# Kernel tuning notes

Measured on AMD Instinct MI355X. Metric: run time of the kernel, lower is better.

Reference implementation:

```python
import jax, jax.numpy as jnp
import numpy as np

N = 20000        # atoms
NEIGH = 12       # neighbors per atom
BSTEPS = 40      # bond GBF steps, range [0, 8]
ASTEPS = 20      # angle GBF steps, range [-1, 1]
H = 64           # hidden size
NCLS = 2         # n_classification
NCRYS = 20       # crystals (contiguous blocks of 1000 atoms)
NREL = 3         # edge relation types


def gbf(data, dmin, dmax, steps):
    # Gaussian basis expansion: exp(-(d - mu)^2 / gamma^2), gamma = (max-min)/steps
    filters = jnp.linspace(dmin, dmax, steps)
    gamma = (dmax - dmin) / steps
    return jnp.exp(-((data[..., None] - filters) ** 2) / gamma ** 2)


def rgcn(x, src, dst, etype, W_rel, W_root, b):
    # RGCNConv (PyG default): out = x @ W_root + b + sum_r mean_{j in N_r(i)} x_j @ W_r
    out = x @ W_root + b
    for r in range(NREL):
        w = (etype == r).astype(x.dtype)                     # [E]
        msg = (x @ W_rel[r])[src] * w[:, None]               # transform-then-gather: [E, H]
        s = jax.ops.segment_sum(msg, dst, num_segments=x.shape[0])
        c = jax.ops.segment_sum(w, dst, num_segments=x.shape[0])
        out = out + s / jnp.maximum(c, 1.0)[:, None]
    return out


def _forward(bond_fea, angle_fea, species, nbr_idx, crys_idx,
             W1b_rel, W1b_root, b1b, W1a_rel, W1a_root, b1a,
             W2b_rel, W2b_root, b2b, W2a_rel, W2a_root, b2a,
             fc_W, fc_b):
    n = bond_fea.shape[0]
    src = jnp.repeat(jnp.arange(n, dtype=jnp.int32), NEIGH)  # edge sources
    dst = nbr_idx.reshape(-1)                                # edge targets
    etype = species[src] + species[dst]                      # 0/1/2 per species pair

    edge_fea = gbf(bond_fea, 0.0, 8.0, BSTEPS).reshape(n, -1)      # [N, 480]
    ang_fea = gbf(angle_fea, -1.0, 1.0, ASTEPS).reshape(n, -1)     # [N, 2880]

    bf = jax.nn.relu(rgcn(edge_fea, src, dst, etype, W1b_rel, W1b_root, b1b))
    af = jax.nn.relu(rgcn(ang_fea, src, dst, etype, W1a_rel, W1a_root, b1a))
    # dropout treated as identity (eval/deterministic reference)
    bf = jax.nn.relu(rgcn(bf, src, dst, etype, W2b_rel, W2b_root, b2b))
    af = jax.nn.relu(rgcn(af, src, dst, etype, W2a_rel, W2a_root, b2a))

    feat = jnp.concatenate([bf, af], axis=1)                 # [N, 128]

    # pool: mean over contiguous [start, end) ranges per crystal
    starts = crys_idx[:, 0]
    crys_id = jnp.searchsorted(starts, jnp.arange(n), side='right') - 1
    sums = jax.ops.segment_sum(feat, crys_id, num_segments=NCRYS)
    counts = (crys_idx[:, 1] - crys_idx[:, 0]).astype(feat.dtype)[:, None]
    pooled = sums / counts                                   # [NCRYS, 128]

    return pooled @ fc_W + fc_b                              # [NCRYS, NCLS]


def setup_inputs() -> dict:
    key = jax.random.key(0)
    ks = jax.random.split(key, 20)
    bond_fea = jax.random.uniform(ks[0], (N, NEIGH), dtype=jnp.float32) * 8.0
    angle_fea = jax.random.uniform(ks[1], (N, NEIGH, NEIGH), dtype=jnp.float32) * 2.0 - 1.0
    species = jax.random.randint(ks[2], (N,), 0, 2, dtype=jnp.int32)
    nbr_idx = jax.random.randint(ks[3], (N, NEIGH), 0, N, dtype=jnp.int32)
    starts = jnp.arange(NCRYS, dtype=jnp.int32) * (N // NCRYS)
    crys_idx = jnp.stack([starts, starts + (N // NCRYS)], axis=1)

    def w(k, shape, fan_in):
        return jax.random.normal(k, shape, dtype=jnp.float32) / np.sqrt(fan_in)

    in_b = BSTEPS * NEIGH            # 480
    in_a = ASTEPS * NEIGH * NEIGH    # 2880
    return {
        'bond_fea': bond_fea, 'angle_fea': angle_fea, 'species': species,
        'nbr_idx': nbr_idx, 'crys_idx': crys_idx,
        'W1b_rel': w(ks[4], (NREL, in_b, H), in_b), 'W1b_root': w(ks[5], (in_b, H), in_b),
        'b1b': jnp.zeros((H,), jnp.float32),
        'W1a_rel': w(ks[6], (NREL, in_a, H), in_a), 'W1a_root': w(ks[7], (in_a, H), in_a),
        'b1a': jnp.zeros((H,), jnp.float32),
        'W2b_rel': w(ks[8], (NREL, H, H), H), 'W2b_root': w(ks[9], (H, H), H),
        'b2b': jnp.zeros((H,), jnp.float32),
        'W2a_rel': w(ks[10], (NREL, H, H), H), 'W2a_root': w(ks[11], (H, H), H),
        'b2a': jnp.zeros((H,), jnp.float32),
        'fc_W': w(ks[12], (2 * H, NCLS), 2 * H), 'fc_b': jnp.zeros((NCLS,), jnp.float32),
    }


def reference(bond_fea, angle_fea, species, nbr_idx, crys_idx,
              W1b_rel, W1b_root, b1b, W1a_rel, W1a_root, b1a,
              W2b_rel, W2b_root, b2b, W2a_rel, W2a_root, b2a,
              fc_W, fc_b):
    return _forward(bond_fea, angle_fea, species, nbr_idx, crys_idx,
                    W1b_rel, W1b_root, b1b, W1a_rel, W1a_root, b1a,
                    W2b_rel, W2b_root, b2b, W2a_rel, W2a_root, b2a,
                    fc_W, fc_b)
```

## Files before the change

kernel.cpp:

```cpp
#include <hip/hip_runtime.h>

#define NN 20000
#define NNP 20096
#define NEIGH 12
#define NCRYS 20
#define MT2 1256
#define NSUB 16

typedef __bf16 bf16x8 __attribute__((ext_vector_type(8)));
typedef __bf16 bf16x4 __attribute__((ext_vector_type(4)));
typedef float f32x4 __attribute__((ext_vector_type(4)));

__device__ __forceinline__ void pack_one(const float* Wrel, const float* Wroot,
                                         __bf16* Wp, int K, int idx) {
    int k = idx >> 8, n = idx & 255;
    int r = n >> 6, h = n & 63;
    float v = (r < 3) ? Wrel[((size_t)r * K + k) * 64 + h] : Wroot[(size_t)k * 64 + h];
    int kt = k >> 5, k8 = (k >> 3) & 3, j = k & 7, nt = n >> 4, ni = n & 15;
    Wp[((((size_t)kt * 16 + nt) * 4 + k8) * 16 + ni) * 8 + j] = (__bf16)v;
}

__device__ __forceinline__ void pack_cat(const float* Wrel, const float* Wroot,
                                         __bf16* Wp, int idx) {
    int k4 = idx >> 6, n = idx & 63;
    int q = k4 >> 6, kk = k4 & 63;
    float v = q ? Wrel[(((q - 1) * 64 + kk) * 64) + n] : Wroot[kk * 64 + n];
    int kt = k4 >> 5, k8 = (k4 >> 3) & 3, j = k4 & 7, nt = n >> 4, ni = n & 15;
    Wp[((((size_t)kt * 4 + nt) * 4 + k8) * 16 + ni) * 8 + j] = (__bf16)v;
}

__global__ __launch_bounds__(256) void setup_kernel(
    const int* __restrict__ species, const int* __restrict__ nbr,
    int* __restrict__ adj, int* __restrict__ deg,
    const float* __restrict__ W1b_rel, const float* __restrict__ W1b_root,
    const float* __restrict__ W1a_rel, const float* __restrict__ W1a_root,
    const float* __restrict__ W2b_rel, const float* __restrict__ W2b_root,
    const float* __restrict__ W2a_rel, const float* __restrict__ W2a_root,
    __bf16* __restrict__ Wp1b, __bf16* __restrict__ Wp1a,
    __bf16* __restrict__ Wp2b, __bf16* __restrict__ Wp2a,
    const float* __restrict__ bond, const float* __restrict__ angle,
    float* __restrict__ bondT, float* __restrict__ angleT) {
    __shared__ float ls[64 * 145];
    const int bx = blockIdx.x, tid = threadIdx.x;
    if (bx < 938) {
        int e = bx * 256 + tid;
        if (e < NN * NEIGH) {
            int i = e / NEIGH;
            int d = nbr[e];
            int r = species[i] + species[d];
            int slot = atomicAdd(&deg[d], 1);
            if (slot < 64) adj[(size_t)d * 64 + slot] = i | (r << 28);
        }
    } else if (bx < 938 + 256) {
        const int S0 = 480 * 256;
        const int S1 = S0 + 2880 * 256;
        const int S2 = S1 + 16384;
        const int S3 = S2 + 16384;
        const int S4 = S3 + 8192;
        const int S5 = S4 + 16384;
        for (int idx = (bx - 938) * 256 + tid; idx < S5; idx += 256 * 256) {
            if (idx < S0)       pack_one(W1b_rel, W1b_root, Wp1b, 480, idx);
            else if (idx < S1)  pack_one(W1a_rel, W1a_root, Wp1a, 2880, idx - S0);
            else if (idx < S2)  pack_cat(W2b_rel, W2b_root, Wp2b, idx - S1);
            else if (idx < S3)  pack_cat(W2a_rel, W2a_root, Wp2a, idx - S2);
            else if (idx < S4)  Wp1b[480 * 256 + (idx - S3)] = (__bf16)0.f;
            else                Wp1a[2880 * 256 + (idx - S4)] = (__bf16)0.f;
        }
    } else {
        int tb = bx - 1194;
        if (tb < 314) {
            int m0 = tb * 64;
            for (int idx = tid; idx < 64 * 144; idx += 256) {
                int mm = idx / 144, j = idx - mm * 144;
                int m = m0 + mm;
                ls[mm * 145 + j] = (m < NN) ? angle[(size_t)m * 144 + j] : 0.f;
            }
            __syncthreads();
            for (int idx = tid; idx < 148 * 64; idx += 256) {
                int j = idx >> 6, mm = idx & 63;
                angleT[(size_t)j * NNP + m0 + mm] = (j < 144) ? ls[mm * 145 + j] : 0.f;
            }
        } else {
            int m0 = (tb - 314) * 64;
            for (int idx = tid; idx < 64 * 12; idx += 256) {
                int mm = idx / 12, j = idx - mm * 12;
                int m = m0 + mm;
                ls[mm * 13 + j] = (m < NN) ? bond[(size_t)m * 12 + j] : 0.f;
            }
            __syncthreads();
            for (int idx = tid; idx < 16 * 64; idx += 256) {
                int j = idx >> 6, mm = idx & 63;
                bondT[(size_t)j * NNP + m0 + mm] = (j < 12) ? ls[mm * 13 + j] : 0.f;
            }
        }
    }
}

template <int MODE>
__device__ __forceinline__ void gemm1_body(const float* __restrict__ xT,
                                           const __bf16* __restrict__ Wp,
                                           __bf16* __restrict__ Y, int mb,
                                           __bf16* __restrict__ Al) {
    constexpr int KTOT = (MODE == 0) ? 512 : 2944;
    constexpr int NPH = KTOT / 64;
    constexpr int DIVN = (MODE == 0) ? 40 : 20;
    constexpr int ADDJ = 64 / DIVN;
    constexpr int ADDS = 64 % DIVN;
    constexpr float F0 = (MODE == 0) ? 0.f : -1.f;
    constexpr float FS = (MODE == 0) ? (8.f / 39.f) : (2.f / 19.f);
    constexpr float NG2 = ((MODE == 0) ? -25.f : -100.f) * 1.44269504f;
    const float C  = __builtin_amdgcn_exp2f(2.f * NG2 * FS * FS);
    const float P1 = NG2 * FS * FS;
    const float P2 = -2.f * NG2 * FS;

    const int tid = threadIdx.x;
    const int lane = tid & 63, wv = tid >> 6;
    const int m0 = mb * 64;
    const int smt = tid >> 7;
    const int sk8 = (tid >> 5) & 3;
    const int smi = (tid >> 1) & 15;
    const int sjh = (tid & 1) * 4;
    const int sgm = m0 + smt * 16 + smi;
    const int kk0 = sk8 * 8 + sjh;
    const int swoff = (((smt * 4 + sk8) * 16 + smi) * 8 + sjh);
    const int k8b = lane >> 4, nib = lane & 15;

    f32x4 acc[4][2] = {};

    const float* pA0 = xT + (size_t)(kk0 / DIVN) * NNP + sgm;
    const float* pA1 = xT + (size_t)((32 + kk0) / DIVN) * NNP + sgm;
    int sL0 = kk0 % DIVN, sL1 = (32 + kk0) % DIVN;
    int sS0 = sL0, sS1 = sL1;

    const bf16x8* pB0 = (const bf16x8*)Wp + ((size_t)(2 * wv) * 4 + k8b) * 16 + nib;
    const bf16x8* pB1 = pB0 + 1024;

    bf16x8 bEv[4], bOd[4];

    auto advL = [&]() {
        sL0 += ADDS;
        if (sL0 >= DIVN) { sL0 -= DIVN; pA0 += (size_t)(ADDJ + 1) * NNP; } else pA0 += (size_t)ADDJ * NNP;
        sL1 += ADDS;
        if (sL1 >= DIVN) { sL1 -= DIVN; pA1 += (size_t)(ADDJ + 1) * NNP; } else pA1 += (size_t)ADDJ * NNP;
    };
    auto advS = [&]() {
        sS0 += ADDS; if (sS0 >= DIVN) sS0 -= DIVN;
        sS1 += ADDS; if (sS1 >= DIVN) sS1 -= DIVN;
    };
    auto loadB = [&](bf16x8* d) {
        d[0] = pB0[0]; d[1] = pB0[64]; d[2] = pB1[0]; d[3] = pB1[64];
        pB0 += 2048; pB1 += 2048;
    };
    auto stage = [&](float a0, float a1, __bf16* dst) {
        float d0 = a0 - (F0 + (float)sS0 * FS);
        float d1 = a1 - (F0 + (float)sS1 * FS);
        float e0a = __builtin_amdgcn_exp2f(NG2 * d0 * d0);
        float q0a = __builtin_amdgcn_exp2f(fmaf(P2, d0, P1));
        float e0b = __builtin_amdgcn_exp2f(NG2 * d1 * d1);
        float q0b = __builtin_amdgcn_exp2f(fmaf(P2, d1, P1));
        float e1a = e0a * q0a, q1a = q0a * C;
        float e2a = e1a * q1a, e3a = e2a * q1a * C;
        float e1b = e0b * q0b, q1b = q0b * C;
        float e2b = e1b * q1b, e3b = e2b * q1b * C;
        bf16x4 v0, v1;
        v0[0] = (__bf16)e0a; v0[1] = (__bf16)e1a; v0[2] = (__bf16)e2a; v0[3] = (__bf16)e3a;
        v1[0] = (__bf16)e0b; v1[1] = (__bf16)e1b; v1[2] = (__bf16)e2b; v1[3] = (__bf16)e3b;
        *(bf16x4*)&dst[swoff] = v0;
        *(bf16x4*)&dst[2048 + swoff] = v1;
    };
    auto mma = [&](const __bf16* Ab, const bf16x8* bc) {
        bf16x8 af[4], ag[4];
#pragma unroll
        for (int t4 = 0; t4 < 4; ++t4) {
            af[t4] = *(const bf16x8*)&Ab[(((((t4 << 2) + k8b) << 4) + nib) << 3)];
            ag[t4] = *(const bf16x8*)&Ab[2048 + (((((t4 << 2) + k8b) << 4) + nib) << 3)];
        }
#pragma unroll
        for (int i = 0; i < 4; ++i) {
            acc[i][0] = __builtin_amdgcn_mfma_f32_16x16x32_bf16(af[i], bc[0], acc[i][0], 0, 0, 0);
            acc[i][1] = __builtin_amdgcn_mfma_f32_16x16x32_bf16(af[i], bc[1], acc[i][1], 0, 0, 0);
        }
#pragma unroll
        for (int i = 0; i < 4; ++i) {
            acc[i][0] = __builtin_amdgcn_mfma_f32_16x16x32_bf16(ag[i], bc[2], acc[i][0], 0, 0, 0);
            acc[i][1] = __builtin_amdgcn_mfma_f32_16x16x32_bf16(ag[i], bc[3], acc[i][1], 0, 0, 0);
        }
    };

    float a00 = pA0[0], a01 = pA1[0]; advL();
    float aN0 = pA0[0], aN1 = pA1[0]; advL();
    stage(a00, a01, Al); advS();
    loadB(bEv);
    loadB(bOd);
    __syncthreads();

    for (int p2 = 0; p2 < NPH / 2; ++p2) {
        const bool last = (p2 == NPH / 2 - 1);
        mma(Al, bEv);
        if (!last) loadB(bEv);
        stage(aN0, aN1, Al + 4096); advS();
        if (!last) { aN0 = pA0[0]; aN1 = pA1[0]; advL(); }
        __syncthreads();
        mma(Al + 4096, bOd);
        if (!last) {
            loadB(bOd);
            stage(aN0, aN1, Al); advS();
            aN0 = pA0[0]; aN1 = pA1[0]; advL();
        }
        __syncthreads();
    }

    const int mrow0 = m0 + ((lane >> 4) << 2);
    const int ncol = (wv << 5) + nib;
#pragma unroll
    for (int i = 0; i < 4; ++i)
#pragma unroll
        for (int j = 0; j < 2; ++j)
#pragma unroll
            for (int v = 0; v < 4; ++v) {
                int m = mrow0 + i * 16 + v;
                if (m < NN) Y[(size_t)m * 256 + ncol + j * 16] = (__bf16)acc[i][j][v];
            }
}

__global__ __launch_bounds__(512, 4) void mega_gemm1(const float* __restrict__ bondT,
                                                     const float* __restrict__ angleT,
                                                     const __bf16* __restrict__ Wp1b,
                                                     const __bf16* __restrict__ Wp1a,
                                                     __bf16* __restrict__ Yb, __bf16* __restrict__ Ya) {
    __shared__ __align__(16) __bf16 Al[2 * 4096];
    int bx = blockIdx.x;
    if (bx < 314) gemm1_body<1>(angleT, Wp1a, Ya, bx, Al);
    else          gemm1_body<0>(bondT, Wp1b, Yb, bx - 314, Al);
}

__device__ __forceinline__ float agg_node(const __bf16* __restrict__ Y,
                                          const int* __restrict__ adj,
                                          const int* __restrict__ deg,
                                          const float* __restrict__ bias,
                                          int node, int h) {
    int dg = min(deg[node], 64);
    int e = adj[(size_t)node * 64 + h];
    bool val = h < dg;
    int r = e >> 28;
    unsigned long long bl0 = __ballot(val && r == 0);
    unsigned long long bl1 = __ballot(val && r == 1);
    unsigned long long bl2 = __ballot(val && r == 2);
    int c0 = __popcll(bl0), c1 = __popcll(bl1), c2 = __popcll(bl2);
    float s0 = 0.f, s1 = 0.f, s2 = 0.f;
    if (dg > 0) {
        int e0 = __builtin_amdgcn_readfirstlane(e);
        int ec = val ? e : e0;
        for (int k0 = 0; k0 < dg; k0 += 16) {
            float v[16];
#pragma unroll
            for (int i = 0; i < 16; ++i) {
                int ek = __builtin_amdgcn_readlane(ec, k0 + i);
                v[i] = (float)Y[(size_t)(ek & 0x0FFFFFFF) * 256 + (ek >> 28) * 64 + h];
            }
#pragma unroll
            for (int i = 0; i < 16; ++i) {
                int kk = k0 + i;
                if (kk < dg) {
                    int rr = __builtin_amdgcn_readlane(ec, kk) >> 28;
                    if (rr == 0) s0 += v[i];
                    else if (rr == 1) s1 += v[i];
                    else s2 += v[i];
                }
            }
        }
    }
    float o = (float)Y[(size_t)node * 256 + 192 + h] + bias[h] +
              s0 / fmaxf((float)c0, 1.f) + s1 / fmaxf((float)c1, 1.f) +
              s2 / fmaxf((float)c2, 1.f);
    return fmaxf(o, 0.f);
}

__global__ __launch_bounds__(256) void agg_packed(const __bf16* __restrict__ Yb,
                                                  const __bf16* __restrict__ Ya,
                                                  const int* __restrict__ adj,
                                                  const int* __restrict__ deg,
                                                  const float* __restrict__ biasb,
                                                  const float* __restrict__ biasa,
                                                  __bf16* __restrict__ outb,
                                                  __bf16* __restrict__ outa) {
    const __bf16* Y = blockIdx.y ? Ya : Yb;
    const float* bias = blockIdx.y ? biasa : biasb;
    __bf16* outp = blockIdx.y ? outa : outb;
    int node = blockIdx.x * 4 + (threadIdx.x >> 6);
    int h = threadIdx.x & 63;
    if (node >= NN) return;
    float o = agg_node(Y, adj, deg, bias, node, h);
    outp[(size_t)node * 64 + h] = (__bf16)o;
}

__global__ __launch_bounds__(256) void agg2(const __bf16* __restrict__ Hb,
                                            const __bf16* __restrict__ Ha,
                                            const int* __restrict__ adj,
                                            const int* __restrict__ deg,
                                            __bf16* __restrict__ Apb,
                                            __bf16* __restrict__ Apa) {
    const __bf16* H = blockIdx.y ? Ha : Hb;
    __bf16* Ap = blockIdx.y ? Apa : Apb;
    int node = blockIdx.x * 4 + (threadIdx.x >> 6);
    int h = threadIdx.x & 63;
    float hd = 0.f, r0 = 0.f, r1 = 0.f, r2 = 0.f;
    if (node < NN) {
        int dg = min(deg[node], 64);
        int e = adj[(size_t)node * 64 + h];
        bool val = h < dg;
        int r = e >> 28;
        unsigned long long bl0 = __ballot(val && r == 0);
        unsigned long long bl1 = __ballot(val && r == 1);
        unsigned long long bl2 = __ballot(val && r == 2);
        int c0 = __popcll(bl0), c1 = __popcll(bl1), c2 = __popcll(bl2);
        float s0 = 0.f, s1 = 0.f, s2 = 0.f;
        hd = (float)H[(size_t)node * 64 + h];
        if (dg > 0) {
            int e0 = __builtin_amdgcn_readfirstlane(e);
            int ec = val ? e : e0;
            for (int k0 = 0; k0 < dg; k0 += 16) {
                float v[16];
#pragma unroll
                for (int i = 0; i < 16; ++i) {
                    int ek = __builtin_amdgcn_readlane(ec, k0 + i);
                    v[i] = (float)H[(size_t)(ek & 0x0FFFFFFF) * 64 + h];
                }
#pragma unroll
                for (int i = 0; i < 16; ++i) {
                    int kk = k0 + i;
                    if (kk < dg) {
                        int rr = __builtin_amdgcn_readlane(ec, kk) >> 28;
                        if (rr == 0) s0 += v[i];
                        else if (rr == 1) s1 += v[i];
                        else s2 += v[i];
                    }
                }
            }
        }
        r0 = s0 / fmaxf((float)c0, 1.f);
        r1 = s1 / fmaxf((float)c1, 1.f);
        r2 = s2 / fmaxf((float)c2, 1.f);
    }
    int mt = node >> 4, mi = node & 15;
    float vals[4] = {hd, r0, r1, r2};
#pragma unroll
    for (int q = 0; q < 4; ++q) {
        int K4 = q * 64 + h;
        int kt = K4 >> 5, k8 = (K4 >> 3) & 3, j = K4 & 7;
        Ap[((((size_t)kt * MT2 + mt) * 4 + k8) * 16 + mi) * 8 + j] = (__bf16)vals[q];
    }
}

__global__ __launch_bounds__(256) void gemm3(const __bf16* __restrict__ Apb,
                                             const __bf16* __restrict__ Apa,
                                             const __bf16* __restrict__ Wpb,
                                             const __bf16* __restrict__ Wpa,
                                             const float* __restrict__ bb,
                                             const float* __restrict__ ba,
                                             const int* __restrict__ crys,
                                             float* __restrict__ pooled) {
    const int ch = blockIdx.y;
    const bf16x8* Ag = (const bf16x8*)(ch ? Apa : Apb);
    const bf16x8* Bg = (const bf16x8*)(ch ? Wpa : Wpb);
    const float* bias = ch ? ba : bb;
    const int base = ch ? 64 : 0;
    const int tid = threadIdx.x, lane = tid & 63, wv = tid >> 6;
    const int mt0 = blockIdx.x * 8 + wv * 2;
    const int k8b = lane >> 4, nib = lane & 15;
    f32x4 acc[2][4] = {};
#pragma unroll
    for (int kt = 0; kt < 8; ++kt) {
        bf16x8 a0 = Ag[(((size_t)kt * MT2 + mt0) * 4 + k8b) * 16 + nib];
        bf16x8 a1 = Ag[(((size_t)kt * MT2 + mt0 + 1) * 4 + k8b) * 16 + nib];
        bf16x8 b0 = Bg[(((size_t)kt * 4 + 0) * 4 + k8b) * 16 + nib];
        bf16x8 b1 = Bg[(((size_t)kt * 4 + 1) * 4 + k8b) * 16 + nib];
        bf16x8 b2 = Bg[(((size_t)kt * 4 + 2) * 4 + k8b) * 16 + nib];
        bf16x8 b3 = Bg[(((size_t)kt * 4 + 3) * 4 + k8b) * 16 + nib];
        acc[0][0] = __builtin_amdgcn_mfma_f32_16x16x32_bf16(a0, b0, acc[0][0], 0, 0, 0);
        acc[0][1] = __builtin_amdgcn_mfma_f32_16x16x32_bf16(a0, b1, acc[0][1], 0, 0, 0);
        acc[0][2] = __builtin_amdgcn_mfma_f32_16x16x32_bf16(a0, b2, acc[0][2], 0, 0, 0);
        acc[0][3] = __builtin_amdgcn_mfma_f32_16x16x32_bf16(a0, b3, acc[0][3], 0, 0, 0);
        acc[1][0] = __builtin_amdgcn_mfma_f32_16x16x32_bf16(a1, b0, acc[1][0], 0, 0, 0);
        acc[1][1] = __builtin_amdgcn_mfma_f32_16x16x32_bf16(a1, b1, acc[1][1], 0, 0, 0);
        acc[1][2] = __builtin_amdgcn_mfma_f32_16x16x32_bf16(a1, b2, acc[1][2], 0, 0, 0);
        acc[1][3] = __builtin_amdgcn_mfma_f32_16x16x32_bf16(a1, b3, acc[1][3], 0, 0, 0);
    }
    const int rowoff = ((lane >> 4) << 2);
#pragma unroll
    for (int i = 0; i < 2; ++i)
#pragma unroll
        for (int v = 0; v < 4; ++v) {
            int m = (mt0 + i) * 16 + rowoff + v;
            if (m < NN) {
                int cc = 0;
#pragma unroll
                for (int t = 1; t < NCRYS; ++t) cc += (m >= crys[t * 2]) ? 1 : 0;
                int sub = ((m >> 4) + ((m >> 2) & 3)) & (NSUB - 1);
                float* pb = &pooled[((size_t)cc * NSUB + sub) * 128 + base];
#pragma unroll
                for (int j = 0; j < 4; ++j) {
                    int n = j * 16 + nib;
                    float o = fmaxf(acc[i][j][v] + bias[n], 0.f);
                    atomicAdd(&pb[n], o);
                }
            }
        }
}

__global__ void final2(const float* __restrict__ pooled, const int* __restrict__ crys,
                       const float* __restrict__ fcW, const float* __restrict__ fcb,
                       float* __restrict__ out) {
    int c = blockIdx.x >> 1, o = blockIdx.x & 1;
    int l = threadIdx.x;
    float cnt = (float)(crys[c * 2 + 1] - crys[c * 2]);
    float sb = 0.f, sa = 0.f;
    for (int s = 0; s < NSUB; ++s) {
        sb += pooled[((size_t)c * NSUB + s) * 128 + l];
        sa += pooled[((size_t)c * NSUB + s) * 128 + 64 + l];
    }
    float a = sb * fcW[l * 2 + o] + sa * fcW[(64 + l) * 2 + o];
    for (int s = 32; s > 0; s >>= 1) a += __shfl_down(a, s);
    if (l == 0) out[c * 2 + o] = a / cnt + fcb[o];
}

extern "C" void kernel_launch(void* const* d_in, const int* in_sizes, int n_in,
                              void* d_out, int out_size, void* d_ws, size_t ws_size,
                              hipStream_t stream) {
    const float* bond    = (const float*)d_in[0];
    const float* angle   = (const float*)d_in[1];
    const int*   species = (const int*)d_in[2];
    const int*   nbr     = (const int*)d_in[3];
    const int*   crys    = (const int*)d_in[4];
    const float* W1b_rel = (const float*)d_in[5];
    const float* W1b_root= (const float*)d_in[6];
    const float* b1b     = (const float*)d_in[7];
    const float* W1a_rel = (const float*)d_in[8];
    const float* W1a_root= (const float*)d_in[9];
    const float* b1a     = (const float*)d_in[10];
    const float* W2b_rel = (const float*)d_in[11];
    const float* W2b_root= (const float*)d_in[12];
    const float* b2b     = (const float*)d_in[13];
    const float* W2a_rel = (const float*)d_in[14];
    const float* W2a_root= (const float*)d_in[15];
    const float* b2a     = (const float*)d_in[16];
    const float* fcW     = (const float*)d_in[17];
    const float* fcb     = (const float*)d_in[18];
    float* out = (float*)d_out;

    char* ws = (char*)d_ws;
    size_t off = 0;
    auto alloc = [&](size_t bytes) {
        char* p = ws + off;
        off = (off + bytes + 255) & ~(size_t)255;
        return p;
    };
    __bf16* Wp1b = (__bf16*)alloc((size_t)512 * 256 * 2);
    __bf16* Wp1a = (__bf16*)alloc((size_t)2944 * 256 * 2);
    __bf16* Wp2b = (__bf16*)alloc((size_t)256 * 64 * 2);
    __bf16* Wp2a = (__bf16*)alloc((size_t)256 * 64 * 2);
    float*  bondT = (float*)alloc((size_t)16 * NNP * 4);
    float*  angleT= (float*)alloc((size_t)148 * NNP * 4);
    __bf16* Yb   = (__bf16*)alloc((size_t)NN * 256 * 2);
    __bf16* Ya   = (__bf16*)alloc((size_t)NN * 256 * 2);
    __bf16* Hrowb= (__bf16*)alloc((size_t)NNP * 64 * 2);
    __bf16* Hrowa= (__bf16*)alloc((size_t)NNP * 64 * 2);
    __bf16* Apb  = (__bf16*)alloc((size_t)8 * MT2 * 512 * 2);
    __bf16* Apa  = (__bf16*)alloc((size_t)8 * MT2 * 512 * 2);
    int*    adj  = (int*)alloc((size_t)NN * 64 * 4);
    int*    deg  = (int*)alloc((size_t)NN * 4);
    float*  pooled = (float*)alloc((size_t)NCRYS * NSUB * 128 * 4);

    hipMemsetAsync(deg, 0, (size_t)NN * 4, stream);
    hipMemsetAsync(pooled, 0, (size_t)NCRYS * NSUB * 128 * 4, stream);

    setup_kernel<<<1822, 256, 0, stream>>>(species, nbr, adj, deg,
                                           W1b_rel, W1b_root, W1a_rel, W1a_root,
                                           W2b_rel, W2b_root, W2a_rel, W2a_root,
                                           Wp1b, Wp1a, Wp2b, Wp2a,
                                           bond, angle, bondT, angleT);

    mega_gemm1<<<628, 512, 0, stream>>>(bondT, angleT, Wp1b, Wp1a, Yb, Ya);
    agg_packed<<<dim3(5024, 2), 256, 0, stream>>>(Yb, Ya, adj, deg, b1b, b1a, Hrowb, Hrowa);
    agg2<<<dim3(5024, 2), 256, 0, stream>>>(Hrowb, Hrowa, adj, deg, Apb, Apa);
    gemm3<<<dim3(157, 2), 256, 0, stream>>>(Apb, Apa, Wp2b, Wp2a, b2b, b2a, crys, pooled);
    final2<<<NCRYS * 2, 64, 0, stream>>>(pooled, crys, fcW, fcb, out);
}
```

Measured before the change: 251.9 us.

## Retile gemm1 to 4 waves with 64x64 per-wave tiles and merge bond/angle aggregation

The first-layer GEMM now runs 256 threads per block, and each wave computes a 64x64 output tile (4x4 MFMA accumulators) instead of 64x32. This raises MFMA work per A-fragment load and per LDS read. The B fragments are loaded per phase rather than double-buffered in registers. Each thread also computes four Gaussian-expanded A values per phase. Both aggregation kernels now process the bond and angle channels in one block, sharing the adjacency reads, ballots and readlanes and halving the grid. The cost is higher register pressure from 16 accumulators and less overlap of B loads with compute.

```diff
diff --git a/kernel.cpp b/kernel.cpp
--- a/kernel.cpp
+++ b/kernel.cpp
@@ -116,114 +116,109 @@
     const int tid = threadIdx.x;
     const int lane = tid & 63, wv = tid >> 6;
     const int m0 = mb * 64;
-    const int smt = tid >> 7;
-    const int sk8 = (tid >> 5) & 3;
-    const int smi = (tid >> 1) & 15;
-    const int sjh = (tid & 1) * 4;
+    const int smi = tid & 15;
+    const int sk8 = (tid >> 4) & 3;
+    const int smt = tid >> 6;
     const int sgm = m0 + smt * 16 + smi;
-    const int kk0 = sk8 * 8 + sjh;
-    const int swoff = (((smt * 4 + sk8) * 16 + smi) * 8 + sjh);
+    const int swbase = ((smt * 4 + sk8) * 16 + smi) * 8;
     const int k8b = lane >> 4, nib = lane & 15;
 
-    f32x4 acc[4][2] = {};
-
-    const float* pA0 = xT + (size_t)(kk0 / DIVN) * NNP + sgm;
-    const float* pA1 = xT + (size_t)((32 + kk0) / DIVN) * NNP + sgm;
-    int sL0 = kk0 % DIVN, sL1 = (32 + kk0) % DIVN;
-    int sS0 = sL0, sS1 = sL1;
-
-    const bf16x8* pB0 = (const bf16x8*)Wp + ((size_t)(2 * wv) * 4 + k8b) * 16 + nib;
-    const bf16x8* pB1 = pB0 + 1024;
-
-    bf16x8 bEv[4], bOd[4];
-
-    auto advL = [&]() {
-        sL0 += ADDS;
-        if (sL0 >= DIVN) { sL0 -= DIVN; pA0 += (size_t)(ADDJ + 1) * NNP; } else pA0 += (size_t)ADDJ * NNP;
-        sL1 += ADDS;
-        if (sL1 >= DIVN) { sL1 -= DIVN; pA1 += (size_t)(ADDJ + 1) * NNP; } else pA1 += (size_t)ADDJ * NNP;
+    f32x4 acc[4][4] = {};
+
+    const float* pAx[4];
+    int sS[4];
+#pragma unroll
+    for (int c = 0; c < 4; ++c) {
+        int k0 = (c >> 1) * 32 + sk8 * 8 + (c & 1) * 4;
+        pAx[c] = xT + (size_t)(k0 / DIVN) * NNP + sgm;
+        sS[c] = k0 % DIVN;
+    }
+    float xv[4];
+
+    auto loadX = [&]() {
+#pragma unroll
+        for (int c = 0; c < 4; ++c) xv[c] = pAx[c][0];
     };
-    auto advS = [&]() {
-        sS0 += ADDS; if (sS0 >= DIVN) sS0 -= DIVN;
-        sS1 += ADDS; if (sS1 >= DIVN) sS1 -= DIVN;
+    auto adv = [&]() {
+#pragma unroll
+        for (int c = 0; c < 4; ++c) {
+            sS[c] += ADDS;
+            if (sS[c] >= DIVN) { sS[c] -= DIVN; pAx[c] += (size_t)(ADDJ + 1) * NNP; }
+            else pAx[c] += (size_t)ADDJ * NNP;
+        }
     };
-    auto loadB = [&](bf16x8* d) {
-        d[0] = pB0[0]; d[1] = pB0[64]; d[2] = pB1[0]; d[3] = pB1[64];
-        pB0 += 2048; pB1 += 2048;
+    auto stage = [&](__bf16* dst) {
+#pragma unroll
+        for (int c = 0; c < 4; ++c) {
+            float d0 = xv[c] - (F0 + (float)sS[c] * FS);
+            float e0 = __builtin_amdgcn_exp2f(NG2 * d0 * d0);
+            float q0 = __builtin_amdgcn_exp2f(fmaf(P2, d0, P1));
+            float e1 = e0 * q0, q1 = q0 * C;
+            float e2 = e1 * q1, e3 = e2 * q1 * C;
+            bf16x4 v;
+            v[0] = (__bf16)e0; v[1] = (__bf16)e1; v[2] = (__bf16)e2; v[3] = (__bf16)e3;
+            *(bf16x4*)&dst[(c >> 1) * 2048 + swbase + (c & 1) * 4] = v;
+        }
     };
-    auto stage = [&](float a0, float a1, __bf16* dst) {
-        float d0 = a0 - (F0 + (float)sS0 * FS);
-        float d1 = a1 - (F0 + (float)sS1 * FS);
-        float e0a = __builtin_amdgcn_exp2f(NG2 * d0 * d0);
-        float q0a = __builtin_amdgcn_exp2f(fmaf(P2, d0, P1));
-        float e0b = __builtin_amdgcn_exp2f(NG2 * d1 * d1);
-        float q0b = __builtin_amdgcn_exp2f(fmaf(P2, d1, P1));
-        float e1a = e0a * q0a, q1a = q0a * C;
-        float e2a = e1a * q1a, e3a = e2a * q1a * C;
-        float e1b = e0b * q0b, q1b = q0b * C;
-        float e2b = e1b * q1b, e3b = e2b * q1b * C;
-        bf16x4 v0, v1;
-        v0[0] = (__bf16)e0a; v0[1] = (__bf16)e1a; v0[2] = (__bf16)e2a; v0[3] = (__bf16)e3a;
-        v1[0] = (__bf16)e0b; v1[1] = (__bf16)e1b; v1[2] = (__bf16)e2b; v1[3] = (__bf16)e3b;
-        *(bf16x4*)&dst[swoff] = v0;
-        *(bf16x4*)&dst[2048 + swoff] = v1;
-    };
-    auto mma = [&](const __bf16* Ab, const bf16x8* bc) {
-        bf16x8 af[4], ag[4];
-#pragma unroll
-        for (int t4 = 0; t4 < 4; ++t4) {
-            af[t4] = *(const bf16x8*)&Ab[(((((t4 << 2) + k8b) << 4) + nib) << 3)];
-            ag[t4] = *(const bf16x8*)&Ab[2048 + (((((t4 << 2) + k8b) << 4) + nib) << 3)];
-        }
-#pragma unroll
-        for (int i = 0; i < 4; ++i) {
-            acc[i][0] = __builtin_amdgcn_mfma_f32_16x16x32_bf16(af[i], bc[0], acc[i][0], 0, 0, 0);
-            acc[i][1] = __builtin_amdgcn_mfma_f32_16x16x32_bf16(af[i], bc[1], acc[i][1], 0, 0, 0);
-        }
-#pragma unroll
-        for (int i = 0; i < 4; ++i) {
-            acc[i][0] = __builtin_amdgcn_mfma_f32_16x16x32_bf16(ag[i], bc[2], acc[i][0], 0, 0, 0);
-            acc[i][1] = __builtin_amdgcn_mfma_f32_16x16x32_bf16(ag[i], bc[3], acc[i][1], 0, 0, 0);
-        }
-    };
-
-    float a00 = pA0[0], a01 = pA1[0]; advL();
-    float aN0 = pA0[0], aN1 = pA1[0]; advL();
-    stage(a00, a01, Al); advS();
-    loadB(bEv);
-    loadB(bOd);
+
+    const bf16x8* pB = (const bf16x8*)Wp + ((size_t)(wv * 16 + k8b)) * 16 + nib;
+
+    loadX();
+    stage(Al);
+    adv();
     __syncthreads();
 
-    for (int p2 = 0; p2 < NPH / 2; ++p2) {
-        const bool last = (p2 == NPH / 2 - 1);
-        mma(Al, bEv);
-        if (!last) loadB(bEv);
-        stage(aN0, aN1, Al + 4096); advS();
-        if (!last) { aN0 = pA0[0]; aN1 = pA1[0]; advL(); }
+    for (int ph = 0; ph < NPH; ++ph) {
+        if (ph + 1 < NPH) loadX();
+        const __bf16* Ab = Al + ((ph & 1) << 12);
+        {
+            bf16x8 bB[4], af[4];
+#pragma unroll
+            for (int jn = 0; jn < 4; ++jn) bB[jn] = pB[jn * 64];
+#pragma unroll
+            for (int mt = 0; mt < 4; ++mt)
+                af[mt] = *(const bf16x8*)&Ab[((mt * 4 + k8b) * 16 + nib) * 8];
+#pragma unroll
+            for (int mt = 0; mt < 4; ++mt)
+#pragma unroll
+                for (int jn = 0; jn < 4; ++jn)
+                    acc[mt][jn] = __builtin_amdgcn_mfma_f32_16x16x32_bf16(af[mt], bB[jn], acc[mt][jn], 0, 0, 0);
+        }
+        {
+            bf16x8 bB[4], af[4];
+#pragma unroll
+            for (int jn = 0; jn < 4; ++jn) bB[jn] = pB[1024 + jn * 64];
+#pragma unroll
+            for (int mt = 0; mt < 4; ++mt)
+                af[mt] = *(const bf16x8*)&Ab[2048 + ((mt * 4 + k8b) * 16 + nib) * 8];
+#pragma unroll
+            for (int mt = 0; mt < 4; ++mt)
+#pragma unroll
+                for (int jn = 0; jn < 4; ++jn)
+                    acc[mt][jn] = __builtin_amdgcn_mfma_f32_16x16x32_bf16(af[mt], bB[jn], acc[mt][jn], 0, 0, 0);
+        }
+        pB += 2048;
+        if (ph + 1 < NPH) {
+            stage(Al + (((ph & 1) ^ 1) << 12));
+            adv();
+        }
         __syncthreads();
-        mma(Al + 4096, bOd);
-        if (!last) {
-            loadB(bOd);
-            stage(aN0, aN1, Al); advS();
-            aN0 = pA0[0]; aN1 = pA1[0]; advL();
-        }
-        __syncthreads();
     }
 
     const int mrow0 = m0 + ((lane >> 4) << 2);
-    const int ncol = (wv << 5) + nib;
-#pragma unroll
-    for (int i = 0; i < 4; ++i)
-#pragma unroll
-        for (int j = 0; j < 2; ++j)
+    const int ncol0 = wv * 64 + nib;
+#pragma unroll
+    for (int mt = 0; mt < 4; ++mt)
+#pragma unroll
+        for (int jn = 0; jn < 4; ++jn)
 #pragma unroll
             for (int v = 0; v < 4; ++v) {
-                int m = mrow0 + i * 16 + v;
-                if (m < NN) Y[(size_t)m * 256 + ncol + j * 16] = (__bf16)acc[i][j][v];
-            }
-}
-
-__global__ __launch_bounds__(512, 4) void mega_gemm1(const float* __restrict__ bondT,
+                int m = mrow0 + mt * 16 + v;
+                if (m < NN) Y[(size_t)m * 256 + ncol0 + jn * 16] = (__bf16)acc[mt][jn][v];
+            }
+}
+
+__global__ __launch_bounds__(256, 4) void mega_gemm1(const float* __restrict__ bondT,
                                                      const float* __restrict__ angleT,
                                                      const __bf16* __restrict__ Wp1b,
                                                      const __bf16* __restrict__ Wp1a,
@@ -234,11 +229,17 @@
     else          gemm1_body<0>(bondT, Wp1b, Yb, bx - 314, Al);
 }
 
-__device__ __forceinline__ float agg_node(const __bf16* __restrict__ Y,
-                                          const int* __restrict__ adj,
-                                          const int* __restrict__ deg,
-                                          const float* __restrict__ bias,
-                                          int node, int h) {
+__global__ __launch_bounds__(256) void agg1(const __bf16* __restrict__ Yb,
+                                            const __bf16* __restrict__ Ya,
+                                            const int* __restrict__ adj,
+                                            const int* __restrict__ deg,
+                                            const float* __restrict__ biasb,
+                                            const float* __restrict__ biasa,
+                                            __bf16* __restrict__ Hb,
+                                            __bf16* __restrict__ Ha) {
+    int node = blockIdx.x * 4 + (threadIdx.x >> 6);
+    int h = threadIdx.x & 63;
+    if (node >= NN) return;
     int dg = min(deg[node], 64);
     int e = adj[(size_t)node * 64 + h];
     bool val = h < dg;
@@ -247,51 +248,39 @@
     unsigned long long bl1 = __ballot(val && r == 1);
     unsigned long long bl2 = __ballot(val && r == 2);
     int c0 = __popcll(bl0), c1 = __popcll(bl1), c2 = __popcll(bl2);
-    float s0 = 0.f, s1 = 0.f, s2 = 0.f;
+    float sb0 = 0.f, sb1 = 0.f, sb2 = 0.f;
+    float sa0 = 0.f, sa1 = 0.f, sa2 = 0.f;
     if (dg > 0) {
         int e0 = __builtin_amdgcn_readfirstlane(e);
         int ec = val ? e : e0;
         for (int k0 = 0; k0 < dg; k0 += 16) {
-            float v[16];
+            float vb[16], va[16];
 #pragma unroll
             for (int i = 0; i < 16; ++i) {
                 int ek = __builtin_amdgcn_readlane(ec, k0 + i);
-                v[i] = (float)Y[(size_t)(ek & 0x0FFFFFFF) * 256 + (ek >> 28) * 64 + h];
+                size_t base = (size_t)(ek & 0x0FFFFFFF) * 256 + (ek >> 28) * 64 + h;
+                vb[i] = (float)Yb[base];
+                va[i] = (float)Ya[base];
             }
 #pragma unroll
             for (int i = 0; i < 16; ++i) {
                 int kk = k0 + i;
                 if (kk < dg) {
                     int rr = __builtin_amdgcn_readlane(ec, kk) >> 28;
-                    if (rr == 0) s0 += v[i];
-                    else if (rr == 1) s1 += v[i];
-                    else s2 += v[i];
+                    if (rr == 0)      { sb0 += vb[i]; sa0 += va[i]; }
+                    else if (rr == 1) { sb1 += vb[i]; sa1 += va[i]; }
+                    else              { sb2 += vb[i]; sa2 += va[i]; }
                 }
             }
         }
     }
-    float o = (float)Y[(size_t)node * 256 + 192 + h] + bias[h] +
-              s0 / fmaxf((float)c0, 1.f) + s1 / fmaxf((float)c1, 1.f) +
-              s2 / fmaxf((float)c2, 1.f);
-    return fmaxf(o, 0.f);
-}
-
-__global__ __launch_bounds__(256) void agg_packed(const __bf16* __restrict__ Yb,
-                                                  const __bf16* __restrict__ Ya,
-                                                  const int* __restrict__ adj,
-                                                  const int* __restrict__ deg,
-                                                  const float* __restrict__ biasb,
-                                                  const float* __restrict__ biasa,
-                                                  __bf16* __restrict__ outb,
-                                                  __bf16* __restrict__ outa) {
-    const __bf16* Y = blockIdx.y ? Ya : Yb;
-    const float* bias = blockIdx.y ? biasa : biasb;
-    __bf16* outp = blockIdx.y ? outa : outb;
-    int node = blockIdx.x * 4 + (threadIdx.x >> 6);
-    int h = threadIdx.x & 63;
-    if (node >= NN) return;
-    float o = agg_node(Y, adj, deg, bias, node, h);
-    outp[(size_t)node * 64 + h] = (__bf16)o;
+    float i0 = 1.f / fmaxf((float)c0, 1.f);
+    float i1 = 1.f / fmaxf((float)c1, 1.f);
+    float i2 = 1.f / fmaxf((float)c2, 1.f);
+    float ob = (float)Yb[(size_t)node * 256 + 192 + h] + biasb[h] + sb0 * i0 + sb1 * i1 + sb2 * i2;
+    float oa = (float)Ya[(size_t)node * 256 + 192 + h] + biasa[h] + sa0 * i0 + sa1 * i1 + sa2 * i2;
+    Hb[(size_t)node * 64 + h] = (__bf16)fmaxf(ob, 0.f);
+    Ha[(size_t)node * 64 + h] = (__bf16)fmaxf(oa, 0.f);
 }
 
 __global__ __launch_bounds__(256) void agg2(const __bf16* __restrict__ Hb,
@@ -300,11 +289,10 @@
                                             const int* __restrict__ deg,
                                             __bf16* __restrict__ Apb,
                                             __bf16* __restrict__ Apa) {
-    const __bf16* H = blockIdx.y ? Ha : Hb;
-    __bf16* Ap = blockIdx.y ? Apa : Apb;
     int node = blockIdx.x * 4 + (threadIdx.x >> 6);
     int h = threadIdx.x & 63;
-    float hd = 0.f, r0 = 0.f, r1 = 0.f, r2 = 0.f;
+    float hb = 0.f, rb0 = 0.f, rb1 = 0.f, rb2 = 0.f;
+    float ha = 0.f, ra0 = 0.f, ra1 = 0.f, ra2 = 0.f;
     if (node < NN) {
         int dg = min(deg[node], 64);
         int e = adj[(size_t)node * 64 + h];
@@ -314,41 +302,50 @@
         unsigned long long bl1 = __ballot(val && r == 1);
         unsigned long long bl2 = __ballot(val && r == 2);
         int c0 = __popcll(bl0), c1 = __popcll(bl1), c2 = __popcll(bl2);
-        float s0 = 0.f, s1 = 0.f, s2 = 0.f;
-        hd = (float)H[(size_t)node * 64 + h];
+        float sb0 = 0.f, sb1 = 0.f, sb2 = 0.f;
+        float sa0 = 0.f, sa1 = 0.f, sa2 = 0.f;
+        hb = (float)Hb[(size_t)node * 64 + h];
+        ha = (float)Ha[(size_t)node * 64 + h];
         if (dg > 0) {
             int e0 = __builtin_amdgcn_readfirstlane(e);
             int ec = val ? e : e0;
             for (int k0 = 0; k0 < dg; k0 += 16) {
-                float v[16];
+                float vb[16], va[16];
 #pragma unroll
                 for (int i = 0; i < 16; ++i) {
                     int ek = __builtin_amdgcn_readlane(ec, k0 + i);
-                    v[i] = (float)H[(size_t)(ek & 0x0FFFFFFF) * 64 + h];
+                    size_t base = (size_t)(ek & 0x0FFFFFFF) * 64 + h;
+                    vb[i] = (float)Hb[base];
+                    va[i] = (float)Ha[base];
                 }
 #pragma unroll
                 for (int i = 0; i < 16; ++i) {
                     int kk = k0 + i;
                     if (kk < dg) {
                         int rr = __builtin_amdgcn_readlane(ec, kk) >> 28;
-                        if (rr == 0) s0 += v[i];
-                        else if (rr == 1) s1 += v[i];
-                        else s2 += v[i];
+                        if (rr == 0)      { sb0 += vb[i]; sa0 += va[i]; }
+                        else if (rr == 1) { sb1 += vb[i]; sa1 += va[i]; }
+                        else              { sb2 += vb[i]; sa2 += va[i]; }
                     }
                 }
             }
         }
-        r0 = s0 / fmaxf((float)c0, 1.f);
-        r1 = s1 / fmaxf((float)c1, 1.f);
-        r2 = s2 / fmaxf((float)c2, 1.f);
+        float i0 = 1.f / fmaxf((float)c0, 1.f);
+        float i1 = 1.f / fmaxf((float)c1, 1.f);
+        float i2 = 1.f / fmaxf((float)c2, 1.f);
+        rb0 = sb0 * i0; rb1 = sb1 * i1; rb2 = sb2 * i2;
+        ra0 = sa0 * i0; ra1 = sa1 * i1; ra2 = sa2 * i2;
     }
     int mt = node >> 4, mi = node & 15;
-    float vals[4] = {hd, r0, r1, r2};
+    float vb4[4] = {hb, rb0, rb1, rb2};
+    float va4[4] = {ha, ra0, ra1, ra2};
 #pragma unroll
     for (int q = 0; q < 4; ++q) {
         int K4 = q * 64 + h;
         int kt = K4 >> 5, k8 = (K4 >> 3) & 3, j = K4 & 7;
-        Ap[((((size_t)kt * MT2 + mt) * 4 + k8) * 16 + mi) * 8 + j] = (__bf16)vals[q];
+        size_t off = ((((size_t)kt * MT2 + mt) * 4 + k8) * 16 + mi) * 8 + j;
+        Apb[off] = (__bf16)vb4[q];
+        Apa[off] = (__bf16)va4[q];
     }
 }
 
@@ -480,9 +477,9 @@
                                            Wp1b, Wp1a, Wp2b, Wp2a,
                                            bond, angle, bondT, angleT);
 
-    mega_gemm1<<<628, 512, 0, stream>>>(bondT, angleT, Wp1b, Wp1a, Yb, Ya);
-    agg_packed<<<dim3(5024, 2), 256, 0, stream>>>(Yb, Ya, adj, deg, b1b, b1a, Hrowb, Hrowa);
-    agg2<<<dim3(5024, 2), 256, 0, stream>>>(Hrowb, Hrowa, adj, deg, Apb, Apa);
+    mega_gemm1<<<628, 256, 0, stream>>>(bondT, angleT, Wp1b, Wp1a, Yb, Ya);
+    agg1<<<5024, 256, 0, stream>>>(Yb, Ya, adj, deg, b1b, b1a, Hrowb, Hrowa);
+    agg2<<<5024, 256, 0, stream>>>(Hrowb, Hrowa, adj, deg, Apb, Apa);
     gemm3<<<dim3(157, 2), 256, 0, stream>>>(Apb, Apa, Wp2b, Wp2a, b2b, b2a, crys, pooled);
     final2<<<NCRYS * 2, 64, 0, stream>>>(pooled, crys, fcW, fcb, out);
 }
```

Result: faster. 240.1 us (-4.7%).

## Split angle GEMM over K into two halves and fuse bond/angle aggregation kernels

Applied to the files above, without the earlier changes.

The angle GEMM's K dimension is padded to 3072 and split across two block groups, each writing fp32 partial results. A new addY kernel sums the partials and converts them to bf16. This raises the block count for the dominant long-K GEMM to reduce tail imbalance, at the cost of extra fp32 traffic and one more launch. The bond and angle aggregation passes are also merged into single kernels that gather both feature sets per edge, so adjacency reads and ballot work are shared.

```diff
diff --git a/kernel.cpp b/kernel.cpp
--- a/kernel.cpp
+++ b/kernel.cpp
@@ -57,7 +57,7 @@
         const int S2 = S1 + 16384;
         const int S3 = S2 + 16384;
         const int S4 = S3 + 8192;
-        const int S5 = S4 + 16384;
+        const int S5 = S4 + 49152;
         for (int idx = (bx - 938) * 256 + tid; idx < S5; idx += 256 * 256) {
             if (idx < S0)       pack_one(W1b_rel, W1b_root, Wp1b, 480, idx);
             else if (idx < S1)  pack_one(W1a_rel, W1a_root, Wp1a, 2880, idx - S0);
@@ -76,7 +76,7 @@
                 ls[mm * 145 + j] = (m < NN) ? angle[(size_t)m * 144 + j] : 0.f;
             }
             __syncthreads();
-            for (int idx = tid; idx < 148 * 64; idx += 256) {
+            for (int idx = tid; idx < 156 * 64; idx += 256) {
                 int j = idx >> 6, mm = idx & 63;
                 angleT[(size_t)j * NNP + m0 + mm] = (j < 144) ? ls[mm * 145 + j] : 0.f;
             }
@@ -96,13 +96,12 @@
     }
 }
 
-template <int MODE>
+template <int MODE, typename OUT_T>
 __device__ __forceinline__ void gemm1_body(const float* __restrict__ xT,
                                            const __bf16* __restrict__ Wp,
-                                           __bf16* __restrict__ Y, int mb,
-                                           __bf16* __restrict__ Al) {
-    constexpr int KTOT = (MODE == 0) ? 512 : 2944;
-    constexpr int NPH = KTOT / 64;
+                                           OUT_T* __restrict__ Y, int mb,
+                                           __bf16* __restrict__ Al,
+                                           int ph0, int nph) {
     constexpr int DIVN = (MODE == 0) ? 40 : 20;
     constexpr int ADDJ = 64 / DIVN;
     constexpr int ADDS = 64 % DIVN;
@@ -127,12 +126,15 @@
 
     f32x4 acc[4][2] = {};
 
-    const float* pA0 = xT + (size_t)(kk0 / DIVN) * NNP + sgm;
-    const float* pA1 = xT + (size_t)((32 + kk0) / DIVN) * NNP + sgm;
-    int sL0 = kk0 % DIVN, sL1 = (32 + kk0) % DIVN;
+    const int k00 = ph0 * 64 + kk0;
+    const int k01 = ph0 * 64 + 32 + kk0;
+    const float* pA0 = xT + (size_t)(k00 / DIVN) * NNP + sgm;
+    const float* pA1 = xT + (size_t)(k01 / DIVN) * NNP + sgm;
+    int sL0 = k00 % DIVN, sL1 = k01 % DIVN;
     int sS0 = sL0, sS1 = sL1;
 
-    const bf16x8* pB0 = (const bf16x8*)Wp + ((size_t)(2 * wv) * 4 + k8b) * 16 + nib;
+    const bf16x8* pB0 = (const bf16x8*)Wp + (size_t)ph0 * 2048 +
+                        ((size_t)(2 * wv) * 4 + k8b) * 16 + nib;
     const bf16x8* pB1 = pB0 + 1024;
 
     bf16x8 bEv[4], bOd[4];
@@ -194,8 +196,9 @@
     loadB(bOd);
     __syncthreads();
 
-    for (int p2 = 0; p2 < NPH / 2; ++p2) {
-        const bool last = (p2 == NPH / 2 - 1);
+    const int np2 = nph >> 1;
+    for (int p2 = 0; p2 < np2; ++p2) {
+        const bool last = (p2 == np2 - 1);
         mma(Al, bEv);
         if (!last) loadB(bEv);
         stage(aN0, aN1, Al + 4096); advS();
@@ -219,7 +222,7 @@
 #pragma unroll
             for (int v = 0; v < 4; ++v) {
                 int m = mrow0 + i * 16 + v;
-                if (m < NN) Y[(size_t)m * 256 + ncol + j * 16] = (__bf16)acc[i][j][v];
+                if (m < NN) Y[(size_t)m * 256 + ncol + j * 16] = (OUT_T)acc[i][j][v];
             }
 }
 
@@ -227,18 +230,42 @@
                                                      const float* __restrict__ angleT,
                                                      const __bf16* __restrict__ Wp1b,
                                                      const __bf16* __restrict__ Wp1a,
-                                                     __bf16* __restrict__ Yb, __bf16* __restrict__ Ya) {
+                                                     __bf16* __restrict__ Yb,
+                                                     float* __restrict__ Ya1,
+                                                     float* __restrict__ Ya2) {
     __shared__ __align__(16) __bf16 Al[2 * 4096];
     int bx = blockIdx.x;
-    if (bx < 314) gemm1_body<1>(angleT, Wp1a, Ya, bx, Al);
-    else          gemm1_body<0>(bondT, Wp1b, Yb, bx - 314, Al);
-}
-
-__device__ __forceinline__ float agg_node(const __bf16* __restrict__ Y,
-                                          const int* __restrict__ adj,
-                                          const int* __restrict__ deg,
-                                          const float* __restrict__ bias,
-                                          int node, int h) {
+    if (bx < 314)       gemm1_body<1, float>(angleT, Wp1a, Ya1, bx, Al, 0, 24);
+    else if (bx < 628)  gemm1_body<1, float>(angleT, Wp1a, Ya2, bx - 314, Al, 24, 24);
+    else                gemm1_body<0, __bf16>(bondT, Wp1b, Yb, bx - 628, Al, 0, 8);
+}
+
+__global__ __launch_bounds__(256) void addY(const float* __restrict__ Y1,
+                                            const float* __restrict__ Y2,
+                                            __bf16* __restrict__ Yo) {
+    size_t i = ((size_t)blockIdx.x * 256 + threadIdx.x) * 8;
+    f32x4 a0 = *(const f32x4*)&Y1[i], a1 = *(const f32x4*)&Y1[i + 4];
+    f32x4 b0 = *(const f32x4*)&Y2[i], b1 = *(const f32x4*)&Y2[i + 4];
+    bf16x8 o;
+#pragma unroll
+    for (int c = 0; c < 4; ++c) {
+        o[c] = (__bf16)(a0[c] + b0[c]);
+        o[4 + c] = (__bf16)(a1[c] + b1[c]);
+    }
+    *(bf16x8*)&Yo[i] = o;
+}
+
+__global__ __launch_bounds__(256) void agg1(const __bf16* __restrict__ Yb,
+                                            const __bf16* __restrict__ Ya,
+                                            const int* __restrict__ adj,
+                                            const int* __restrict__ deg,
+                                            const float* __restrict__ biasb,
+                                            const float* __restrict__ biasa,
+                                            __bf16* __restrict__ Hb,
+                                            __bf16* __restrict__ Ha) {
+    int node = blockIdx.x * 4 + (threadIdx.x >> 6);
+    int h = threadIdx.x & 63;
+    if (node >= NN) return;
     int dg = min(deg[node], 64);
     int e = adj[(size_t)node * 64 + h];
     bool val = h < dg;
@@ -247,51 +274,39 @@
     unsigned long long bl1 = __ballot(val && r == 1);
     unsigned long long bl2 = __ballot(val && r == 2);
     int c0 = __popcll(bl0), c1 = __popcll(bl1), c2 = __popcll(bl2);
-    float s0 = 0.f, s1 = 0.f, s2 = 0.f;
+    float sb0 = 0.f, sb1 = 0.f, sb2 = 0.f;
+    float sa0 = 0.f, sa1 = 0.f, sa2 = 0.f;
     if (dg > 0) {
         int e0 = __builtin_amdgcn_readfirstlane(e);
         int ec = val ? e : e0;
         for (int k0 = 0; k0 < dg; k0 += 16) {
-            float v[16];
+            float vb[16], va[16];
 #pragma unroll
             for (int i = 0; i < 16; ++i) {
                 int ek = __builtin_amdgcn_readlane(ec, k0 + i);
-                v[i] = (float)Y[(size_t)(ek & 0x0FFFFFFF) * 256 + (ek >> 28) * 64 + h];
+                size_t base = (size_t)(ek & 0x0FFFFFFF) * 256 + (ek >> 28) * 64 + h;
+                vb[i] = (float)Yb[base];
+                va[i] = (float)Ya[base];
             }
 #pragma unroll
             for (int i = 0; i < 16; ++i) {
                 int kk = k0 + i;
                 if (kk < dg) {
                     int rr = __builtin_amdgcn_readlane(ec, kk) >> 28;
-                    if (rr == 0) s0 += v[i];
-                    else if (rr == 1) s1 += v[i];
-                    else s2 += v[i];
+                    if (rr == 0)      { sb0 += vb[i]; sa0 += va[i]; }
+                    else if (rr == 1) { sb1 += vb[i]; sa1 += va[i]; }
+                    else              { sb2 += vb[i]; sa2 += va[i]; }
                 }
             }
         }
     }
-    float o = (float)Y[(size_t)node * 256 + 192 + h] + bias[h] +
-              s0 / fmaxf((float)c0, 1.f) + s1 / fmaxf((float)c1, 1.f) +
-              s2 / fmaxf((float)c2, 1.f);
-    return fmaxf(o, 0.f);
-}
-
-__global__ __launch_bounds__(256) void agg_packed(const __bf16* __restrict__ Yb,
-                                                  const __bf16* __restrict__ Ya,
-                                                  const int* __restrict__ adj,
-                                                  const int* __restrict__ deg,
-                                                  const float* __restrict__ biasb,
-                                                  const float* __restrict__ biasa,
-                                                  __bf16* __restrict__ outb,
-                                                  __bf16* __restrict__ outa) {
-    const __bf16* Y = blockIdx.y ? Ya : Yb;
-    const float* bias = blockIdx.y ? biasa : biasb;
-    __bf16* outp = blockIdx.y ? outa : outb;
-    int node = blockIdx.x * 4 + (threadIdx.x >> 6);
-    int h = threadIdx.x & 63;
-    if (node >= NN) return;
-    float o = agg_node(Y, adj, deg, bias, node, h);
-    outp[(size_t)node * 64 + h] = (__bf16)o;
+    float i0 = 1.f / fmaxf((float)c0, 1.f);
+    float i1 = 1.f / fmaxf((float)c1, 1.f);
+    float i2 = 1.f / fmaxf((float)c2, 1.f);
+    float ob = (float)Yb[(size_t)node * 256 + 192 + h] + biasb[h] + sb0 * i0 + sb1 * i1 + sb2 * i2;
+    float oa = (float)Ya[(size_t)node * 256 + 192 + h] + biasa[h] + sa0 * i0 + sa1 * i1 + sa2 * i2;
+    Hb[(size_t)node * 64 + h] = (__bf16)fmaxf(ob, 0.f);
+    Ha[(size_t)node * 64 + h] = (__bf16)fmaxf(oa, 0.f);
 }
 
 __global__ __launch_bounds__(256) void agg2(const __bf16* __restrict__ Hb,
@@ -300,11 +315,10 @@
                                             const int* __restrict__ deg,
                                             __bf16* __restrict__ Apb,
                                             __bf16* __restrict__ Apa) {
-    const __bf16* H = blockIdx.y ? Ha : Hb;
-    __bf16* Ap = blockIdx.y ? Apa : Apb;
     int node = blockIdx.x * 4 + (threadIdx.x >> 6);
     int h = threadIdx.x & 63;
-    float hd = 0.f, r0 = 0.f, r1 = 0.f, r2 = 0.f;
+    float hb = 0.f, rb0 = 0.f, rb1 = 0.f, rb2 = 0.f;
+    float ha = 0.f, ra0 = 0.f, ra1 = 0.f, ra2 = 0.f;
     if (node < NN) {
         int dg = min(deg[node], 64);
         int e = adj[(size_t)node * 64 + h];
@@ -314,41 +328,50 @@
         unsigned long long bl1 = __ballot(val && r == 1);
         unsigned long long bl2 = __ballot(val && r == 2);
         int c0 = __popcll(bl0), c1 = __popcll(bl1), c2 = __popcll(bl2);
-        float s0 = 0.f, s1 = 0.f, s2 = 0.f;
-        hd = (float)H[(size_t)node * 64 + h];
+        float sb0 = 0.f, sb1 = 0.f, sb2 = 0.f;
+        float sa0 = 0.f, sa1 = 0.f, sa2 = 0.f;
+        hb = (float)Hb[(size_t)node * 64 + h];
+        ha = (float)Ha[(size_t)node * 64 + h];
         if (dg > 0) {
             int e0 = __builtin_amdgcn_readfirstlane(e);
             int ec = val ? e : e0;
             for (int k0 = 0; k0 < dg; k0 += 16) {
-                float v[16];
+                float vb[16], va[16];
 #pragma unroll
                 for (int i = 0; i < 16; ++i) {
                     int ek = __builtin_amdgcn_readlane(ec, k0 + i);
-                    v[i] = (float)H[(size_t)(ek & 0x0FFFFFFF) * 64 + h];
+                    size_t base = (size_t)(ek & 0x0FFFFFFF) * 64 + h;
+                    vb[i] = (float)Hb[base];
+                    va[i] = (float)Ha[base];
                 }
 #pragma unroll
                 for (int i = 0; i < 16; ++i) {
                     int kk = k0 + i;
                     if (kk < dg) {
                         int rr = __builtin_amdgcn_readlane(ec, kk) >> 28;
-                        if (rr == 0) s0 += v[i];
-                        else if (rr == 1) s1 += v[i];
-                        else s2 += v[i];
+                        if (rr == 0)      { sb0 += vb[i]; sa0 += va[i]; }
+                        else if (rr == 1) { sb1 += vb[i]; sa1 += va[i]; }
+                        else              { sb2 += vb[i]; sa2 += va[i]; }
                     }
                 }
             }
         }
-        r0 = s0 / fmaxf((float)c0, 1.f);
-        r1 = s1 / fmaxf((float)c1, 1.f);
-        r2 = s2 / fmaxf((float)c2, 1.f);
+        float i0 = 1.f / fmaxf((float)c0, 1.f);
+        float i1 = 1.f / fmaxf((float)c1, 1.f);
+        float i2 = 1.f / fmaxf((float)c2, 1.f);
+        rb0 = sb0 * i0; rb1 = sb1 * i1; rb2 = sb2 * i2;
+        ra0 = sa0 * i0; ra1 = sa1 * i1; ra2 = sa2 * i2;
     }
     int mt = node >> 4, mi = node & 15;
-    float vals[4] = {hd, r0, r1, r2};
+    float vb4[4] = {hb, rb0, rb1, rb2};
+    float va4[4] = {ha, ra0, ra1, ra2};
 #pragma unroll
     for (int q = 0; q < 4; ++q) {
         int K4 = q * 64 + h;
         int kt = K4 >> 5, k8 = (K4 >> 3) & 3, j = K4 & 7;
-        Ap[((((size_t)kt * MT2 + mt) * 4 + k8) * 16 + mi) * 8 + j] = (__bf16)vals[q];
+        size_t off = ((((size_t)kt * MT2 + mt) * 4 + k8) * 16 + mi) * 8 + j;
+        Apb[off] = (__bf16)vb4[q];
+        Apa[off] = (__bf16)va4[q];
     }
 }
 
@@ -456,13 +479,15 @@
         return p;
     };
     __bf16* Wp1b = (__bf16*)alloc((size_t)512 * 256 * 2);
-    __bf16* Wp1a = (__bf16*)alloc((size_t)2944 * 256 * 2);
+    __bf16* Wp1a = (__bf16*)alloc((size_t)3072 * 256 * 2);
     __bf16* Wp2b = (__bf16*)alloc((size_t)256 * 64 * 2);
     __bf16* Wp2a = (__bf16*)alloc((size_t)256 * 64 * 2);
     float*  bondT = (float*)alloc((size_t)16 * NNP * 4);
-    float*  angleT= (float*)alloc((size_t)148 * NNP * 4);
+    float*  angleT= (float*)alloc((size_t)156 * NNP * 4);
     __bf16* Yb   = (__bf16*)alloc((size_t)NN * 256 * 2);
     __bf16* Ya   = (__bf16*)alloc((size_t)NN * 256 * 2);
+    float*  Ya1  = (float*)alloc((size_t)NN * 256 * 4);
+    float*  Ya2  = (float*)alloc((size_t)NN * 256 * 4);
     __bf16* Hrowb= (__bf16*)alloc((size_t)NNP * 64 * 2);
     __bf16* Hrowa= (__bf16*)alloc((size_t)NNP * 64 * 2);
     __bf16* Apb  = (__bf16*)alloc((size_t)8 * MT2 * 512 * 2);
@@ -480,9 +505,10 @@
                                            Wp1b, Wp1a, Wp2b, Wp2a,
                                            bond, angle, bondT, angleT);
 
-    mega_gemm1<<<628, 512, 0, stream>>>(bondT, angleT, Wp1b, Wp1a, Yb, Ya);
-    agg_packed<<<dim3(5024, 2), 256, 0, stream>>>(Yb, Ya, adj, deg, b1b, b1a, Hrowb, Hrowa);
-    agg2<<<dim3(5024, 2), 256, 0, stream>>>(Hrowb, Hrowa, adj, deg, Apb, Apa);
+    mega_gemm1<<<942, 512, 0, stream>>>(bondT, angleT, Wp1b, Wp1a, Yb, Ya1, Ya2);
+    addY<<<2500, 256, 0, stream>>>(Ya1, Ya2, Ya);
+    agg1<<<5024, 256, 0, stream>>>(Yb, Ya, adj, deg, b1b, b1a, Hrowb, Hrowa);
+    agg2<<<5024, 256, 0, stream>>>(Hrowb, Hrowa, adj, deg, Apb, Apa);
     gemm3<<<dim3(157, 2), 256, 0, stream>>>(Apb, Apa, Wp2b, Wp2a, b2b, b2a, crys, pooled);
     final2<<<NCRYS * 2, 64, 0, stream>>>(pooled, crys, fcW, fcb, out);
 }
```

Result: faster. 236.9 us (-6.0%).
